# Performance work log

Measured on AMD Instinct MI355X. Metric: run time of the kernel, lower is better.

## Reference

```python
import jax, jax.numpy as jnp
import numpy as np

SHIFT, REDUCE = 0, 1
B, T, E, H = 128, 256, 300, 256


def _make_transitions(T, B):
    # Valid left-branching sequence: S, S, (R, S)*, ending with R -> 2T-1 steps.
    t = np.zeros(2 * T - 1, dtype=np.int32)
    t[2::2] = REDUCE
    return np.tile(t[:, None], (1, B))


def setup_inputs() -> dict:
    key = jax.random.key(0)
    ks = jax.random.split(key, 8)
    stdv = 1.0 / np.sqrt(H)
    u = lambda k, shape: jax.random.uniform(k, shape, jnp.float32, -stdv, stdv)
    return {
        "x": jax.random.normal(ks[0], (B, T, E), jnp.float32),
        "transitions": jnp.asarray(_make_transitions(T, B)),
        "Wp": u(ks[1], (E, H)),
        "bp": u(ks[2], (H,)),
        "Wg": u(ks[3], (E, H)),
        "bg": u(ks[4], (H,)),
        "Wr": u(ks[5], (2 * H, 5 * H)),
        "br": u(ks[6], (5 * H,)),
    }


def reference(x, transitions, Wp, bp, Wg, bg, Wr, br):
    Bb, Tt, _ = x.shape
    Hh = Wp.shape[1]
    # buffers: c = proj_x(x); h = sigmoid(proj_x_gate(x)) * tanh(c)
    c_buf = x @ Wp + bp                      # [B, T, H]
    h_buf = jax.nn.sigmoid(x @ Wg + bg) * jnp.tanh(c_buf)
    bidx = jnp.arange(Bb)

    stack_h0 = jnp.zeros((Bb, Tt, Hh), x.dtype)
    stack_c0 = jnp.zeros((Bb, Tt, Hh), x.dtype)
    sp0 = jnp.zeros((Bb,), jnp.int32)        # stack pointer
    bp0 = jnp.full((Bb,), Tt, jnp.int32)     # buffer pointer (pop from end)

    def step(carry, trans):
        sh, sc, sp, bptr = carry
        is_shift = trans == SHIFT            # [B] bool
        # SHIFT: pop last remaining buffer entry
        nbp = jnp.where(is_shift, bptr - 1, bptr)
        src = jnp.maximum(nbp, 0)
        sft_h = h_buf[bidx, src]
        sft_c = c_buf[bidx, src]
        # REDUCE: children = top two stack entries (r = top, l = below)
        ir = jnp.maximum(sp - 1, 0)
        il = jnp.maximum(sp - 2, 0)
        hl, cl = sh[bidx, il], sc[bidx, il]
        hr, cr = sh[bidx, ir], sc[bidx, ir]
        proj = jnp.concatenate([hl, hr], axis=-1) @ Wr + br   # [B, 5H]
        i, fl, fr, g, o = jnp.split(proj, 5, axis=-1)
        c_red = (jax.nn.sigmoid(fl) * cl + jax.nn.sigmoid(fr) * cr
                 + jax.nn.sigmoid(i) * jnp.tanh(g))
        h_red = jax.nn.sigmoid(o) * jnp.tanh(c_red)
        m = is_shift[:, None]
        h_new = jnp.where(m, sft_h, h_red)
        c_new = jnp.where(m, sft_c, c_red)
        pos = jnp.where(is_shift, sp, il)    # push location
        sh = sh.at[bidx, pos].set(h_new)
        sc = sc.at[bidx, pos].set(c_new)
        sp = jnp.where(is_shift, sp + 1, sp - 1)
        return (sh, sc, sp, nbp), None

    (sh, sc, sp, _), _ = jax.lax.scan(step, (stack_h0, stack_c0, sp0, bp0), transitions)
    # root h state = top of stack, h half only
    return sh[bidx, jnp.maximum(sp - 1, 0)]
```

## Files before the change

### kernel.cpp

```cpp
#include <hip/hip_runtime.h>
#include <hip/hip_fp16.h>
#include <math.h>

#define B_ 128
#define T_ 256
#define E_ 300
#define H_ 256
#define N5_ 1280
#define NSTEPS 511
#define DMAX 8

typedef _Float16 half8_t __attribute__((ext_vector_type(8)));
typedef float float4_t __attribute__((ext_vector_type(4)));
typedef int i4v __attribute__((ext_vector_type(4)));
typedef unsigned int u4v __attribute__((ext_vector_type(4)));

__device__ __forceinline__ float sigm_p(float x){ return 1.f/(1.f + expf(-x)); }
__device__ __forceinline__ float sigm(float x){ return __builtin_amdgcn_rcpf(1.f + __expf(-x)); }
__device__ __forceinline__ float ftanh(float x){
  float xc = fminf(15.f, fmaxf(-15.f, x));
  float e = __expf(-2.f*xc);
  return (1.f - e) * __builtin_amdgcn_rcpf(1.f + e);
}

__global__ __launch_bounds__(64) void k0a_scale(const float* __restrict__ Wr,
    float* __restrict__ scales){
  const int n = blockIdx.x, t = threadIdx.x;
  float m = 0.f;
  #pragma unroll
  for (int j=0;j<4;j++) m = fmaxf(m, fabsf(Wr[(size_t)(t+64*j)*N5_ + n]));
  #pragma unroll
  for (int off=32; off; off>>=1) m = fmaxf(m, __shfl_xor(m, off, 64));
  if (t==0) scales[n] = fmaxf(m, 1e-20f) * (1.f/127.f);
}

__global__ __launch_bounds__(256) void k0b_quant(const float* __restrict__ Wr,
    const float* __restrict__ scales, uint4* __restrict__ W4){
  int idx = blockIdx.x*256 + threadIdx.x;
  if (idx >= 20480) return;
  const int f    = idx >> 6;
  const int lane = idx & 63;
  const int w    = f / 80;
  const int r80  = f - w*80;
  const int g    = r80 >> 4;
  const int cg   = (r80 >> 2) & 3;
  const int kc   = r80 & 3;
  const int ml   = lane & 15, quad = lane >> 4;
  const int col  = g*256 + w*64 + cg*16 + ml;
  const float inv = 1.f / scales[col];
  unsigned int d[4];
  #pragma unroll
  for (int r=0; r<4; r++){
    unsigned int acc = 0;
    #pragma unroll
    for (int j=0; j<4; j++){
      const int k = kc*64 + quad*16 + r*4 + j;
      float wv = Wr[(size_t)k*N5_ + col];
      int q = (int)rintf(wv * inv);
      q = q > 127 ? 127 : (q < -127 ? -127 : q);
      acc |= ((unsigned int)(q & 255)) << (8*j);
    }
    d[r] = acc;
  }
  uint4 v; v.x=d[0]; v.y=d[1]; v.z=d[2]; v.w=d[3];
  W4[idx] = v;
}

__global__ __launch_bounds__(256) void k1_proj(
    const float* __restrict__ x, const float* __restrict__ Wp, const float* __restrict__ bp,
    const float* __restrict__ Wg, const float* __restrict__ bg,
    _Float16* __restrict__ h2, _Float16* __restrict__ c2){
  __shared__ __align__(16) _Float16 As [64*32];
  __shared__ __align__(16) _Float16 BsP[64*32];
  __shared__ __align__(16) _Float16 BsG[64*32];
  const int tid = threadIdx.x;
  const int row0 = blockIdx.x * 64;
  const int n0   = blockIdx.y * 64;
  const int wave = tid >> 6, lane = tid & 63;
  const int ml = lane & 15, quad = lane >> 4;
  float4_t accP[4], accG[4];
  #pragma unroll
  for (int i=0;i<4;i++){ accP[i]=(float4_t)(0.f); accG[i]=(float4_t)(0.f); }
  const int ar = tid >> 2, ak = (tid & 3) * 8;
  const int bk = tid >> 3, bn = (tid & 7) * 8;
  for (int kk = 0; kk < E_; kk += 32){
    __syncthreads();
    {
      const float* src = x + (size_t)(row0 + ar)*E_ + kk + ak;
      float v[8];
      #pragma unroll
      for (int q=0;q<2;q++){
        if (kk + ak + q*4 + 4 <= E_){
          float4_t f = *(const float4_t*)(src + q*4);
          v[q*4+0]=f.x; v[q*4+1]=f.y; v[q*4+2]=f.z; v[q*4+3]=f.w;
        } else {
          #pragma unroll
          for (int j=0;j<4;j++){ int kg = kk+ak+q*4+j; v[q*4+j] = (kg<E_) ? src[q*4+j] : 0.f; }
        }
      }
      #pragma unroll
      for (int j=0;j<8;j++) As[ar*32 + ak + j] = (_Float16)v[j];
    }
    {
      const int kg = kk + bk;
      if (kg < E_){
        const float* sp_ = Wp + (size_t)kg*H_ + n0 + bn;
        const float* sg_ = Wg + (size_t)kg*H_ + n0 + bn;
        float4_t p0 = *(const float4_t*)sp_, p1 = *(const float4_t*)(sp_+4);
        float4_t g0 = *(const float4_t*)sg_, g1 = *(const float4_t*)(sg_+4);
        float pv[8]={p0.x,p0.y,p0.z,p0.w,p1.x,p1.y,p1.z,p1.w};
        float gv[8]={g0.x,g0.y,g0.z,g0.w,g1.x,g1.y,g1.z,g1.w};
        #pragma unroll
        for (int j=0;j<8;j++){ BsP[(bn+j)*32+bk]=(_Float16)pv[j]; BsG[(bn+j)*32+bk]=(_Float16)gv[j]; }
      } else {
        #pragma unroll
        for (int j=0;j<8;j++){ BsP[(bn+j)*32+bk]=(_Float16)0.f; BsG[(bn+j)*32+bk]=(_Float16)0.f; }
      }
    }
    __syncthreads();
    half8_t a = *(const half8_t*)&As[(wave*16 + ml)*32 + quad*8];
    #pragma unroll
    for (int nt=0; nt<4; nt++){
      half8_t b1 = *(const half8_t*)&BsP[(nt*16 + ml)*32 + quad*8];
      accP[nt] = __builtin_amdgcn_mfma_f32_16x16x32_f16(a, b1, accP[nt], 0,0,0);
      half8_t b2 = *(const half8_t*)&BsG[(nt*16 + ml)*32 + quad*8];
      accG[nt] = __builtin_amdgcn_mfma_f32_16x16x32_f16(a, b2, accG[nt], 0,0,0);
    }
  }
  #pragma unroll
  for (int nt=0; nt<4; nt++){
    #pragma unroll
    for (int r=0;r<4;r++){
      int row = row0 + wave*16 + quad*4 + r;
      int col = n0 + nt*16 + ml;
      float c = accP[nt][r] + bp[col];
      float g = accG[nt][r] + bg[col];
      float h = sigm_p(g) * tanhf(c);
      size_t o = (size_t)row*H_ + col;
      c2[o] = (_Float16)c;
      h2[o] = (_Float16)h;
    }
  }
}

__global__ __launch_bounds__(256) void k2_rproj(
    const _Float16* __restrict__ h2, const float* __restrict__ Wr, const float* __restrict__ br,
    _Float16* __restrict__ R2){
  __shared__ __align__(16) _Float16 As[64*32];
  __shared__ __align__(16) _Float16 Bs[64*32];
  const int tid = threadIdx.x;
  const int row0 = blockIdx.x*64, n0 = blockIdx.y*64;
  const int wave = tid>>6, lane = tid&63, ml = lane&15, quad = lane>>4;
  float4_t acc[4];
  #pragma unroll
  for (int i=0;i<4;i++) acc[i]=(float4_t)(0.f);
  const int ar = tid>>2, ak = (tid&3)*8;
  const int bk = tid>>3, bn = (tid&7)*8;
  for (int kk=0; kk<H_; kk+=32){
    __syncthreads();
    *(half8_t*)&As[ar*32+ak] = *(const half8_t*)(h2 + (size_t)(row0+ar)*H_ + kk + ak);
    {
      const float* src = Wr + (size_t)(256 + kk + bk)*N5_ + n0 + bn;
      float4_t f0 = *(const float4_t*)src, f1 = *(const float4_t*)(src+4);
      float v[8]={f0.x,f0.y,f0.z,f0.w,f1.x,f1.y,f1.z,f1.w};
      #pragma unroll
      for (int j=0;j<8;j++) Bs[(bn+j)*32+bk] = (_Float16)v[j];
    }
    __syncthreads();
    half8_t a = *(const half8_t*)&As[(wave*16+ml)*32 + quad*8];
    #pragma unroll
    for (int nt=0; nt<4; nt++){
      half8_t b8 = *(const half8_t*)&Bs[(nt*16+ml)*32 + quad*8];
      acc[nt] = __builtin_amdgcn_mfma_f32_16x16x32_f16(a, b8, acc[nt], 0,0,0);
    }
  }
  #pragma unroll
  for (int nt=0; nt<4; nt++){
    #pragma unroll
    for (int r=0;r<4;r++){
      int row = row0 + wave*16 + quad*4 + r;
      int col = n0 + nt*16 + ml;
      R2[(size_t)row*N5_ + col] = (_Float16)(acc[nt][r] + br[col]);
    }
  }
}

#define K3_LDS_BYTES 86016

#define DECL8(g) u4v bf##g##_0_0, bf##g##_0_1, bf##g##_0_2, bf##g##_0_3, \
                     bf##g##_1_0, bf##g##_1_1, bf##g##_1_2, bf##g##_1_3;
#define LOAD8(g) \
  bf##g##_0_0 = wb[((g)*16 + 0)*64]; bf##g##_0_1 = wb[((g)*16 + 1)*64]; \
  bf##g##_0_2 = wb[((g)*16 + 2)*64]; bf##g##_0_3 = wb[((g)*16 + 3)*64]; \
  bf##g##_1_0 = wb[((g)*16 + 4)*64]; bf##g##_1_1 = wb[((g)*16 + 5)*64]; \
  bf##g##_1_2 = wb[((g)*16 + 6)*64]; bf##g##_1_3 = wb[((g)*16 + 7)*64];

#define MFA(ACC, AF, BF) asm("v_mfma_i32_16x16x64_i8 %0, %1, %2, %0" \
    : "+v"(ACC) : "v"(AF), "a"(BF));
#define MFV(ACC, AF, BF) asm("v_mfma_i32_16x16x64_i8 %0, %1, %2, %0" \
    : "+v"(ACC) : "v"(AF), "v"(BF));
#define FENCE_IN2(A0,A1)  asm volatile("s_nop 1" : "+v"(A0), "+v"(A1));
#define FENCE_OUT2(A0,A1) asm volatile("s_nop 7\n\ts_nop 7" : "+v"(A0), "+v"(A1));
#define BARRIER() asm volatile("s_waitcnt lgkmcnt(0)\n\ts_barrier" ::: "memory")

#define GCHAIN2(g, DST) { \
  i4v A0={0,0,0,0}, A1={0,0,0,0}; \
  FENCE_IN2(A0,A1) \
  MFA(A0,af0,bf##g##_0_0) MFA(A1,af0,bf##g##_1_0) \
  MFA(A0,af1,bf##g##_0_1) MFA(A1,af1,bf##g##_1_1) \
  MFA(A0,af2,bf##g##_0_2) MFA(A1,af2,bf##g##_1_2) \
  MFA(A0,af3,bf##g##_0_3) MFA(A1,af3,bf##g##_1_3) \
  FENCE_OUT2(A0,A1) \
  DST = hsel ? A1.x : A0.x; }

#define GCHAIN2_G4(DST) { \
  const u4v og00=lwg4[0],   og01=lwg4[64],  og02=lwg4[128], og03=lwg4[192]; \
  const u4v og10=lwg4[256], og11=lwg4[320], og12=lwg4[384], og13=lwg4[448]; \
  i4v A0={0,0,0,0}, A1={0,0,0,0}; \
  FENCE_IN2(A0,A1) \
  MFV(A0,af0,og00) MFV(A1,af0,og10) \
  MFV(A0,af1,og01) MFV(A1,af1,og11) \
  MFV(A0,af2,og02) MFV(A1,af2,og12) \
  MFV(A0,af3,og03) MFV(A1,af3,og13) \
  FENCE_OUT2(A0,A1) \
  DST = hsel ? A1.x : A0.x; }

#define PAIR_STEP(IDX, RD, WR) { \
  BARRIER(); \
  float a0=(float)pA0, a1=(float)pA1, a2=(float)pA2, a3=(float)pA3, a4=(float)pA4; \
  const float tc = (float)pAc; \
  const u4v* sRD = (const u4v*)(sI8 + (RD)*H_); \
  const u4v af0 = sRD[quad], af1 = sRD[4+quad], af2 = sRD[8+quad], af3 = sRD[12+quad]; \
  { int rrow = 253-(IDX); if (rrow < 0) rrow = 0; \
    const _Float16* rr = R2 + ((size_t)b*T_ + rrow)*N5_ + col; \
    pA0=rr[0]; pA1=rr[256]; pA2=rr[512]; pA3=rr[768]; pA4=rr[1024]; \
    int crow = 252-(IDX); if (crow < 0) crow = 0; \
    pAc = c2[((size_t)b*T_ + crow)*H_ + col]; } \
  int d0,d1,d2,d3,d4; \
  GCHAIN2(0, d0)  a0 += scf0*(float)d0; \
  GCHAIN2(1, d1)  a1 += scf1*(float)d1; \
  GCHAIN2(2, d2)  a2 += scf2*(float)d2; \
  GCHAIN2(3, d3)  a3 += scf3*(float)d3; \
  GCHAIN2_G4(d4)  a4 += scf4*(float)d4; \
  const float cnew = sigm(a1)*cl + sigm(a2)*cr + sigm(a0)*ftanh(a3); \
  const float hnew = sigm(a4)*ftanh(cnew); \
  sI8[(WR)*H_ + col] = (char)(int)rintf(hnew*127.f); \
  cl = cnew; cr = tc; \
}

__global__ __launch_bounds__(512, 2) void k3_scan(
    const int* __restrict__ trans, const _Float16* __restrict__ h2, const _Float16* __restrict__ c2,
    const _Float16* __restrict__ R2, const uint4* __restrict__ W4,
    const float* __restrict__ scales, const float* __restrict__ Wr,
    const float* __restrict__ br, float* __restrict__ out){
  extern __shared__ char smem[];
  u4v*   wlds  = (u4v*)smem;
  float* sh_   = (float*)(smem + 65536);
  float* sc_   = (float*)(smem + 73728);
  char*  sI8   = (char*)(smem + 81920);
  const u4v* sI4 = (const u4v*)(smem + 81920);
  int* trs     = (int*)(smem + 83968);

  const int b = blockIdx.x, tid = threadIdx.x;
  const int lane = tid & 63, w8 = tid >> 6;
  const int quad = (lane >> 4) & 3;
  const int hsel = (lane >> 4) & 1;
  const int col  = (w8 << 5) + (lane & 31);
  const int w4   = w8 >> 1, cg0 = (w8 & 1) * 2;

  const u4v* WB4v = (const u4v*)W4;
  const u4v* wb   = WB4v + ((size_t)w4*80 + cg0*4)*64 + lane;

  DECL8(0) DECL8(1) DECL8(2) DECL8(3)
  LOAD8(0) LOAD8(1) LOAD8(2) LOAD8(3)

  #pragma unroll
  for (int t=0; t<8; t++){
    const int flat = t*512 + tid;
    const int fd   = flat >> 6;
    const int dl   = flat & 63;
    const int w8d  = fd >> 3;
    const int ii   = (fd >> 2) & 1;
    const int kc   = fd & 3;
    const int cg   = (w8d & 1)*2 + ii;
    const int srcf = (w8d >> 1)*80 + 4*16 + cg*4 + kc;
    wlds[flat] = WB4v[(size_t)srcf*64 + dl];
  }
  const u4v* lwg4 = wlds + (size_t)w8*512 + lane;

  const float scf0 = scales[col       ] * (1.f/127.f);
  const float scf1 = scales[col +  256] * (1.f/127.f);
  const float scf2 = scales[col +  512] * (1.f/127.f);
  const float scf3 = scales[col +  768] * (1.f/127.f);
  const float scf4 = scales[col + 1024] * (1.f/127.f);

  trs[tid] = (tid < NSTEPS) ? trans[(size_t)tid*B_ + b] : 1;
  for (int i = tid; i < DMAX*H_; i += 512){ sh_[i]=0.f; sc_[i]=0.f; sI8[i]=0; }

  int myok = 1;
  if (tid < NSTEPS){ int e = (tid>=2 && (tid&1)==0) ? 1 : 0; if (trs[tid]!=e) myok=0; }
  const int ok = __syncthreads_and(myok);

  if (ok){
    const size_t hb = (size_t)b*T_*H_;
    const _Float16 h255 = h2[hb + 255*H_ + col];
    float cl = (float)c2[hb + 255*H_ + col];
    float cr = (float)c2[hb + 254*H_ + col];
    _Float16 pA0,pA1,pA2,pA3,pA4,pAc;
    { const _Float16* rr = R2 + ((size_t)b*T_ + 254)*N5_ + col;
      pA0=rr[0]; pA1=rr[256]; pA2=rr[512]; pA3=rr[768]; pA4=rr[1024];
      pAc = c2[hb + 253*H_ + col]; }
    sI8[col] = (char)(int)rintf((float)h255 * 127.f);
    #pragma unroll 1
    for (int i=0; i<254; i+=2){
      PAIR_STEP(i,   0, 1)
      PAIR_STEP(i+1, 1, 0)
    }
    {
      BARRIER();
      float a0=(float)pA0, a1=(float)pA1, a2=(float)pA2, a3=(float)pA3, a4=(float)pA4;
      const u4v* sRD = (const u4v*)sI8;
      const u4v af0 = sRD[quad], af1 = sRD[4+quad], af2 = sRD[8+quad], af3 = sRD[12+quad];
      int d0,d1,d2,d3,d4;
      GCHAIN2(0, d0)  a0 += scf0*(float)d0;
      GCHAIN2(1, d1)  a1 += scf1*(float)d1;
      GCHAIN2(2, d2)  a2 += scf2*(float)d2;
      GCHAIN2(3, d3)  a3 += scf3*(float)d3;
      GCHAIN2_G4(d4)  a4 += scf4*(float)d4;
      const float cnew = sigm(a1)*cl + sigm(a2)*cr + sigm(a0)*ftanh(a3);
      const float hnew = sigm(a4)*ftanh(cnew);
      if (lane < 32) out[(size_t)b*H_ + col] = hnew;
    }
    return;
  }

  int sp = 0, bptr = T_, prev_src = -1;
  for (int step=0; step<NSTEPS; step++){
    __syncthreads();
    const int tr = trs[step];
    if (tr == 0){
      const int nbp = bptr - 1;
      const int src = nbp > 0 ? nbp : 0;
      const int slot = sp < 0 ? 0 : (sp > DMAX-1 ? DMAX-1 : sp);
      const size_t o = ((size_t)b*T_ + src)*H_ + col;
      const float wh = (float)h2[o], wc = (float)c2[o];
      sh_[slot*H_+col] = wh;
      sc_[slot*H_+col] = wc;
      sI8[slot*H_+col] = (char)(int)rintf(wh * 127.f);
      sp += 1; bptr = nbp; prev_src = src;
    } else {
      int ir = sp-1 > 0 ? sp-1 : 0;
      int il = sp-2 > 0 ? sp-2 : 0;
      ir = ir > DMAX-1 ? DMAX-1 : ir;
      il = il > DMAX-1 ? DMAX-1 : il;
      const int tg = prev_src;
      const float cl = sc_[il*H_+col];
      const float cr = sc_[ir*H_+col];
      const u4v af0 = sI4[il*16 +  0 + quad];
      const u4v af1 = sI4[il*16 +  4 + quad];
      const u4v af2 = sI4[il*16 +  8 + quad];
      const u4v af3 = sI4[il*16 + 12 + quad];
      float a0,a1,a2,a3,a4;
      if (tg >= 0){
        const _Float16* rr = R2 + ((size_t)b*T_ + tg)*N5_ + col;
        a0=(float)rr[0]; a1=(float)rr[256]; a2=(float)rr[512]; a3=(float)rr[768]; a4=(float)rr[1024];
      } else {
        a0=br[col]; a1=br[col+256]; a2=br[col+512]; a3=br[col+768]; a4=br[col+1024];
      }
      int d0,d1,d2,d3,d4;
      GCHAIN2(0, d0)  a0 += scf0*(float)d0;
      GCHAIN2(1, d1)  a1 += scf1*(float)d1;
      GCHAIN2(2, d2)  a2 += scf2*(float)d2;
      GCHAIN2(3, d3)  a3 += scf3*(float)d3;
      GCHAIN2_G4(d4)  a4 += scf4*(float)d4;
      if (tg < 0){
        for (int k=0; k<H_; k++){
          const float hrk = sh_[ir*H_+k];
          const float* wr = Wr + (size_t)(256+k)*N5_ + col;
          a0 += hrk*wr[0]; a1 += hrk*wr[256]; a2 += hrk*wr[512];
          a3 += hrk*wr[768]; a4 += hrk*wr[1024];
        }
      }
      const float cnew = sigm(a1)*cl + sigm(a2)*cr + sigm(a0)*ftanh(a3);
      const float hnew = sigm(a4)*ftanh(cnew);
      const int wq = (int)rintf(hnew * 127.f);
      __syncthreads();
      sh_[il*H_+col] = hnew;
      sc_[il*H_+col] = cnew;
      sI8[il*H_+col] = (char)wq;
      sp -= 1; prev_src = -1;
    }
  }
  __syncthreads();
  int fs = sp-1 > 0 ? sp-1 : 0;
  fs = fs > DMAX-1 ? DMAX-1 : fs;
  if (lane < 32) out[(size_t)b*H_ + col] = sh_[fs*H_+col];
}

extern "C" void kernel_launch(void* const* d_in, const int* in_sizes, int n_in,
                              void* d_out, int out_size, void* d_ws, size_t ws_size,
                              hipStream_t stream){
  const float* x    = (const float*)d_in[0];
  const int*   trn  = (const int*)  d_in[1];
  const float* Wp   = (const float*)d_in[2];
  const float* bp   = (const float*)d_in[3];
  const float* Wg   = (const float*)d_in[4];
  const float* bg   = (const float*)d_in[5];
  const float* Wr   = (const float*)d_in[6];
  const float* br   = (const float*)d_in[7];
  float* out = (float*)d_out;
  char* w = (char*)d_ws;
  _Float16* h2   = (_Float16*)(w);
  _Float16* c2   = (_Float16*)(w + (size_t)16777216);
  _Float16* R2   = (_Float16*)(w + (size_t)33554432);
  uint4*    W4   = (uint4*)   (w + (size_t)117440512);
  float*    scl  = (float*)   (w + (size_t)117768192);

  hipLaunchKernelGGL(k0a_scale, dim3(1280),    dim3(64),  0, stream, Wr, scl);
  hipLaunchKernelGGL(k0b_quant, dim3(80),      dim3(256), 0, stream, Wr, scl, W4);
  hipLaunchKernelGGL(k1_proj,   dim3(512, 4),  dim3(256), 0, stream, x, Wp, bp, Wg, bg, h2, c2);
  hipLaunchKernelGGL(k2_rproj,  dim3(512, 20), dim3(256), 0, stream, h2, Wr, br, R2);
  hipLaunchKernelGGL(k3_scan,   dim3(128),     dim3(512), K3_LDS_BYTES, stream, trn, h2, c2, R2, W4, scl, Wr, br, out);
}
```

Measured before the change: 512.6 us.

## Pre-transpose weights to fp16 and keep A fragments in registers for projections

Adds two prep kernels that convert Wr's right half and Wp/Wg (padded to K=320) to fp16 in column-major layout. The projection GEMMs then drop their LDS staging and barriers: each block loads its A rows into registers once and loops over all output column tiles, reading B fragments directly from global memory. The grid shrinks to 512 blocks per GEMM, which cuts redundant x/h loads and per-tile conversion but lowers parallelism and relies on cache for B reuse. The prep kernels add launches and extra weight traffic.

```diff
diff --git a/kernel.cpp b/kernel.cpp
--- a/kernel.cpp
+++ b/kernel.cpp
@@ -5,6 +5,7 @@
 #define B_ 128
 #define T_ 256
 #define E_ 300
+#define EP_ 320
 #define H_ 256
 #define N5_ 1280
 #define NSTEPS 511
@@ -66,121 +67,119 @@
   W4[idx] = v;
 }
 
+__global__ __launch_bounds__(256) void k0d_wrt(const float* __restrict__ Wr,
+    _Float16* __restrict__ Wr2t){
+  int idx = blockIdx.x*256 + threadIdx.x;
+  const int col = idx >> 8, k = idx & 255;
+  Wr2t[(size_t)col*H_ + k] = (_Float16)Wr[(size_t)(256 + k)*N5_ + col];
+}
+
+__global__ __launch_bounds__(256) void k0e_wpgt(const float* __restrict__ Wp,
+    const float* __restrict__ Wg, _Float16* __restrict__ Wpt,
+    _Float16* __restrict__ Wgt){
+  int idx = blockIdx.x*256 + threadIdx.x;
+  const int kp = idx >> 8, col = idx & 255;
+  const float* src = blockIdx.y ? Wg : Wp;
+  _Float16* dst = blockIdx.y ? Wgt : Wpt;
+  float v = (kp < E_) ? src[(size_t)kp*H_ + col] : 0.f;
+  dst[(size_t)col*EP_ + kp] = (_Float16)v;
+}
+
 __global__ __launch_bounds__(256) void k1_proj(
-    const float* __restrict__ x, const float* __restrict__ Wp, const float* __restrict__ bp,
-    const float* __restrict__ Wg, const float* __restrict__ bg,
+    const float* __restrict__ x, const _Float16* __restrict__ Wpt, const float* __restrict__ bp,
+    const _Float16* __restrict__ Wgt, const float* __restrict__ bg,
     _Float16* __restrict__ h2, _Float16* __restrict__ c2){
-  __shared__ __align__(16) _Float16 As [64*32];
-  __shared__ __align__(16) _Float16 BsP[64*32];
-  __shared__ __align__(16) _Float16 BsG[64*32];
   const int tid = threadIdx.x;
   const int row0 = blockIdx.x * 64;
-  const int n0   = blockIdx.y * 64;
   const int wave = tid >> 6, lane = tid & 63;
   const int ml = lane & 15, quad = lane >> 4;
-  float4_t accP[4], accG[4];
-  #pragma unroll
-  for (int i=0;i<4;i++){ accP[i]=(float4_t)(0.f); accG[i]=(float4_t)(0.f); }
-  const int ar = tid >> 2, ak = (tid & 3) * 8;
-  const int bk = tid >> 3, bn = (tid & 7) * 8;
-  for (int kk = 0; kk < E_; kk += 32){
-    __syncthreads();
-    {
-      const float* src = x + (size_t)(row0 + ar)*E_ + kk + ak;
-      float v[8];
+  const int arow = row0 + wave*16 + ml;
+
+  half8_t a[10];
+  #pragma unroll
+  for (int kk=0; kk<10; kk++){
+    const int k0 = kk*32 + quad*8;
+    float v[8];
+    if (k0 + 8 <= E_){
+      float4_t f0 = *(const float4_t*)(x + (size_t)arow*E_ + k0);
+      float4_t f1 = *(const float4_t*)(x + (size_t)arow*E_ + k0 + 4);
+      v[0]=f0.x; v[1]=f0.y; v[2]=f0.z; v[3]=f0.w;
+      v[4]=f1.x; v[5]=f1.y; v[6]=f1.z; v[7]=f1.w;
+    } else {
       #pragma unroll
-      for (int q=0;q<2;q++){
-        if (kk + ak + q*4 + 4 <= E_){
-          float4_t f = *(const float4_t*)(src + q*4);
-          v[q*4+0]=f.x; v[q*4+1]=f.y; v[q*4+2]=f.z; v[q*4+3]=f.w;
-        } else {
-          #pragma unroll
-          for (int j=0;j<4;j++){ int kg = kk+ak+q*4+j; v[q*4+j] = (kg<E_) ? src[q*4+j] : 0.f; }
-        }
-      }
+      for (int j=0;j<8;j++){ int k=k0+j; v[j] = (k<E_) ? x[(size_t)arow*E_ + k] : 0.f; }
+    }
+    half8_t h;
+    #pragma unroll
+    for (int j=0;j<8;j++) h[j] = (_Float16)v[j];
+    a[kk] = h;
+  }
+
+  for (int ct=0; ct<4; ct++){
+    float4_t accP[4], accG[4];
+    #pragma unroll
+    for (int i=0;i<4;i++){ accP[i]=(float4_t)(0.f); accG[i]=(float4_t)(0.f); }
+    #pragma unroll
+    for (int kk=0; kk<10; kk++){
       #pragma unroll
-      for (int j=0;j<8;j++) As[ar*32 + ak + j] = (_Float16)v[j];
-    }
-    {
-      const int kg = kk + bk;
-      if (kg < E_){
-        const float* sp_ = Wp + (size_t)kg*H_ + n0 + bn;
-        const float* sg_ = Wg + (size_t)kg*H_ + n0 + bn;
-        float4_t p0 = *(const float4_t*)sp_, p1 = *(const float4_t*)(sp_+4);
-        float4_t g0 = *(const float4_t*)sg_, g1 = *(const float4_t*)(sg_+4);
-        float pv[8]={p0.x,p0.y,p0.z,p0.w,p1.x,p1.y,p1.z,p1.w};
-        float gv[8]={g0.x,g0.y,g0.z,g0.w,g1.x,g1.y,g1.z,g1.w};
-        #pragma unroll
-        for (int j=0;j<8;j++){ BsP[(bn+j)*32+bk]=(_Float16)pv[j]; BsG[(bn+j)*32+bk]=(_Float16)gv[j]; }
-      } else {
-        #pragma unroll
-        for (int j=0;j<8;j++){ BsP[(bn+j)*32+bk]=(_Float16)0.f; BsG[(bn+j)*32+bk]=(_Float16)0.f; }
-      }
-    }
-    __syncthreads();
-    half8_t a = *(const half8_t*)&As[(wave*16 + ml)*32 + quad*8];
+      for (int nt=0; nt<4; nt++){
+        const int col = ct*64 + nt*16 + ml;
+        half8_t b1 = *(const half8_t*)(Wpt + (size_t)col*EP_ + kk*32 + quad*8);
+        accP[nt] = __builtin_amdgcn_mfma_f32_16x16x32_f16(a[kk], b1, accP[nt], 0,0,0);
+        half8_t b2 = *(const half8_t*)(Wgt + (size_t)col*EP_ + kk*32 + quad*8);
+        accG[nt] = __builtin_amdgcn_mfma_f32_16x16x32_f16(a[kk], b2, accG[nt], 0,0,0);
+      }
+    }
     #pragma unroll
     for (int nt=0; nt<4; nt++){
-      half8_t b1 = *(const half8_t*)&BsP[(nt*16 + ml)*32 + quad*8];
-      accP[nt] = __builtin_amdgcn_mfma_f32_16x16x32_f16(a, b1, accP[nt], 0,0,0);
-      half8_t b2 = *(const half8_t*)&BsG[(nt*16 + ml)*32 + quad*8];
-      accG[nt] = __builtin_amdgcn_mfma_f32_16x16x32_f16(a, b2, accG[nt], 0,0,0);
-    }
-  }
-  #pragma unroll
-  for (int nt=0; nt<4; nt++){
-    #pragma unroll
-    for (int r=0;r<4;r++){
-      int row = row0 + wave*16 + quad*4 + r;
-      int col = n0 + nt*16 + ml;
-      float c = accP[nt][r] + bp[col];
-      float g = accG[nt][r] + bg[col];
-      float h = sigm_p(g) * tanhf(c);
-      size_t o = (size_t)row*H_ + col;
-      c2[o] = (_Float16)c;
-      h2[o] = (_Float16)h;
+      #pragma unroll
+      for (int r=0;r<4;r++){
+        int row = row0 + wave*16 + quad*4 + r;
+        int col = ct*64 + nt*16 + ml;
+        float c = accP[nt][r] + bp[col];
+        float g = accG[nt][r] + bg[col];
+        float h = sigm_p(g) * tanhf(c);
+        size_t o = (size_t)row*H_ + col;
+        c2[o] = (_Float16)c;
+        h2[o] = (_Float16)h;
+      }
     }
   }
 }
 
 __global__ __launch_bounds__(256) void k2_rproj(
-    const _Float16* __restrict__ h2, const float* __restrict__ Wr, const float* __restrict__ br,
-    _Float16* __restrict__ R2){
-  __shared__ __align__(16) _Float16 As[64*32];
-  __shared__ __align__(16) _Float16 Bs[64*32];
+    const _Float16* __restrict__ h2, const _Float16* __restrict__ Wr2t,
+    const float* __restrict__ br, _Float16* __restrict__ R2){
   const int tid = threadIdx.x;
-  const int row0 = blockIdx.x*64, n0 = blockIdx.y*64;
+  const int row0 = blockIdx.x*64;
   const int wave = tid>>6, lane = tid&63, ml = lane&15, quad = lane>>4;
-  float4_t acc[4];
-  #pragma unroll
-  for (int i=0;i<4;i++) acc[i]=(float4_t)(0.f);
-  const int ar = tid>>2, ak = (tid&3)*8;
-  const int bk = tid>>3, bn = (tid&7)*8;
-  for (int kk=0; kk<H_; kk+=32){
-    __syncthreads();
-    *(half8_t*)&As[ar*32+ak] = *(const half8_t*)(h2 + (size_t)(row0+ar)*H_ + kk + ak);
-    {
-      const float* src = Wr + (size_t)(256 + kk + bk)*N5_ + n0 + bn;
-      float4_t f0 = *(const float4_t*)src, f1 = *(const float4_t*)(src+4);
-      float v[8]={f0.x,f0.y,f0.z,f0.w,f1.x,f1.y,f1.z,f1.w};
+
+  half8_t a[8];
+  #pragma unroll
+  for (int kk=0; kk<8; kk++)
+    a[kk] = *(const half8_t*)(h2 + (size_t)(row0 + wave*16 + ml)*H_ + kk*32 + quad*8);
+
+  for (int ct=0; ct<20; ct++){
+    float4_t acc[4];
+    #pragma unroll
+    for (int i=0;i<4;i++) acc[i]=(float4_t)(0.f);
+    #pragma unroll
+    for (int kk=0; kk<8; kk++){
       #pragma unroll
-      for (int j=0;j<8;j++) Bs[(bn+j)*32+bk] = (_Float16)v[j];
-    }
-    __syncthreads();
-    half8_t a = *(const half8_t*)&As[(wave*16+ml)*32 + quad*8];
+      for (int nt=0; nt<4; nt++){
+        const int col = ct*64 + nt*16 + ml;
+        half8_t b8 = *(const half8_t*)(Wr2t + (size_t)col*H_ + kk*32 + quad*8);
+        acc[nt] = __builtin_amdgcn_mfma_f32_16x16x32_f16(a[kk], b8, acc[nt], 0,0,0);
+      }
+    }
     #pragma unroll
     for (int nt=0; nt<4; nt++){
-      half8_t b8 = *(const half8_t*)&Bs[(nt*16+ml)*32 + quad*8];
-      acc[nt] = __builtin_amdgcn_mfma_f32_16x16x32_f16(a, b8, acc[nt], 0,0,0);
-    }
-  }
-  #pragma unroll
-  for (int nt=0; nt<4; nt++){
-    #pragma unroll
-    for (int r=0;r<4;r++){
-      int row = row0 + wave*16 + quad*4 + r;
-      int col = n0 + nt*16 + ml;
-      R2[(size_t)row*N5_ + col] = (_Float16)(acc[nt][r] + br[col]);
+      #pragma unroll
+      for (int r=0;r<4;r++){
+        int row = row0 + wave*16 + quad*4 + r;
+        int col = ct*64 + nt*16 + ml;
+        R2[(size_t)row*N5_ + col] = (_Float16)(acc[nt][r] + br[col]);
+      }
     }
   }
 }
@@ -310,7 +309,7 @@
     { const _Float16* rr = R2 + ((size_t)b*T_ + 254)*N5_ + col;
       pA0=rr[0]; pA1=rr[256]; pA2=rr[512]; pA3=rr[768]; pA4=rr[1024];
       pAc = c2[hb + 253*H_ + col]; }
-    sI8[col] = (char)(int)rintf((float)h255 * 127.f);
+    if (hsel == 0 || true) sI8[col] = (char)(int)rintf((float)h255 * 127.f);
     #pragma unroll 1
     for (int i=0; i<254; i+=2){
       PAIR_STEP(i,   0, 1)
@@ -415,10 +414,15 @@
   _Float16* R2   = (_Float16*)(w + (size_t)33554432);
   uint4*    W4   = (uint4*)   (w + (size_t)117440512);
   float*    scl  = (float*)   (w + (size_t)117768192);
+  _Float16* Wr2t = (_Float16*)(w + (size_t)117773312);
+  _Float16* Wpt  = (_Float16*)(w + (size_t)118428672);
+  _Float16* Wgt  = (_Float16*)(w + (size_t)118592512);
 
   hipLaunchKernelGGL(k0a_scale, dim3(1280),    dim3(64),  0, stream, Wr, scl);
   hipLaunchKernelGGL(k0b_quant, dim3(80),      dim3(256), 0, stream, Wr, scl, W4);
-  hipLaunchKernelGGL(k1_proj,   dim3(512, 4),  dim3(256), 0, stream, x, Wp, bp, Wg, bg, h2, c2);
-  hipLaunchKernelGGL(k2_rproj,  dim3(512, 20), dim3(256), 0, stream, h2, Wr, br, R2);
+  hipLaunchKernelGGL(k0d_wrt,   dim3(1280),    dim3(256), 0, stream, Wr, Wr2t);
+  hipLaunchKernelGGL(k0e_wpgt,  dim3(320, 2),  dim3(256), 0, stream, Wp, Wg, Wpt, Wgt);
+  hipLaunchKernelGGL(k1_proj,   dim3(512),     dim3(256), 0, stream, x, Wpt, bp, Wgt, bg, h2, c2);
+  hipLaunchKernelGGL(k2_rproj,  dim3(512),     dim3(256), 0, stream, h2, Wr2t, br, R2);
   hipLaunchKernelGGL(k3_scan,   dim3(128),     dim3(512), K3_LDS_BYTES, stream, trn, h2, c2, R2, W4, scl, Wr, br, out);
 }
```

Result: slower. 598.6 us (+16.8%).
